# Kernel optimization log

Measured on AMD Instinct MI355X. Metric: run time of the kernel, lower is better.

Reference implementation:

```python
import jax, jax.numpy as jnp
import numpy as np

B, S, F = 4, 2048, 512
H, DK, DV, FILT = 8, 64, 64, 512

def setup_inputs() -> dict:
    key = jax.random.key(0)
    ks = jax.random.split(key, 11)
    sc_in = 1.0 / np.sqrt(F)
    sc_o = 1.0 / np.sqrt(H * DV)
    return {
        "x_q": jax.random.normal(ks[0], (B, S, F), jnp.float32),
        "x_k": jax.random.normal(ks[1], (B, S, F), jnp.float32),
        "x_v": jax.random.normal(ks[2], (B, S, F), jnp.float32),
        "Wq": jax.random.normal(ks[3], (H, F, DK), jnp.float32) * sc_in,
        "bq": jax.random.normal(ks[4], (H, DK), jnp.float32) * 0.01,
        "Wk": jax.random.normal(ks[5], (H, F, DK), jnp.float32) * sc_in,
        "bk": jax.random.normal(ks[6], (H, DK), jnp.float32) * 0.01,
        "Wv": jax.random.normal(ks[7], (H, F, DV), jnp.float32) * sc_in,
        "bv": jax.random.normal(ks[8], (H, DV), jnp.float32) * 0.01,
        "Wo": jax.random.normal(ks[9], (H * DV, FILT), jnp.float32) * sc_o,
        "bo": jax.random.normal(ks[10], (FILT,), jnp.float32) * 0.01,
    }

def reference(x_q, x_k, x_v, Wq, bq, Wk, bk, Wv, bv, Wo, bo):
    d_k = Wq.shape[-1]
    # per-head Dense projections, batched over heads: [B,H,S,dk/dv]
    q = jnp.einsum("bsf,hfk->bhsk", x_q, Wq) + bq[:, None, :]
    k = jnp.einsum("bsf,hfk->bhsk", x_k, Wk) + bk[:, None, :]
    v = jnp.einsum("bsf,hfv->bhsv", x_v, Wv) + bv[:, None, :]
    # scaled dot-product attention (scale by 1/sqrt(d_k) as in map_fn)
    scores = jnp.einsum("bhsk,bhtk->bhst", q, k) / jnp.sqrt(jnp.asarray(d_k, q.dtype))
    attn = jax.nn.softmax(scores, axis=-1)
    out = jnp.einsum("bhst,bhtv->bhsv", attn, v)
    # concat heads along feature dim -> [B,S,H*DV], then output linear
    bsz, h, s, dv = out.shape
    concat = out.transpose(0, 2, 1, 3).reshape(bsz, s, h * dv)
    return concat @ Wo + bo
```

## Files before the change

kernel.cpp:

```cpp
#include <hip/hip_runtime.h>

#define B_    4
#define S_    2048
#define H_    8
#define M_    (B_ * S_)

typedef __bf16    bf16_t;
typedef _Float16  f16_t;
typedef __bf16   bf16x8 __attribute__((ext_vector_type(8)));
typedef __bf16   bf16x4 __attribute__((ext_vector_type(4)));
typedef _Float16 f16x8  __attribute__((ext_vector_type(8)));
typedef float    f32x16 __attribute__((ext_vector_type(16)));

union B8 { uint4 u; bf16x8 v; bf16_t e[8]; };
union B4 { uint2 u; bf16x4 v; bf16_t e[4]; };
union H8 { uint4 u; f16x8  v; f16_t  e[8]; };
union H4 { uint2 u; f16_t  e[4]; };

#define QSCALE 0.1803368801111204f

typedef const __attribute__((address_space(1))) unsigned int ga_u32;
typedef __attribute__((address_space(3))) unsigned int       ls_u32;
__device__ __forceinline__ void g2l16(const void* g, void* l) {
    __builtin_amdgcn_global_load_lds((ga_u32*)g, (ls_u32*)l, 16, 0, 0);
}

__global__ __launch_bounds__(256) void prep(
    const float* __restrict__ xq, const float* __restrict__ xk,
    const float* __restrict__ xv,
    bf16_t* __restrict__ dq, bf16_t* __restrict__ dk, bf16_t* __restrict__ dv,
    const float* __restrict__ w0, const float* __restrict__ w1,
    const float* __restrict__ w2, const float* __restrict__ wo,
    bf16_t* __restrict__ t0, bf16_t* __restrict__ t1,
    bf16_t* __restrict__ t2, f16_t* __restrict__ wot)
{
    __shared__ float T[64][65];
    const int bid = blockIdx.x;
    const int tid = threadIdx.x;

    if (bid < 3072) {
        const int z  = bid >> 10;
        const int bx = bid & 1023;
        const float* src = z == 0 ? xq : z == 1 ? xk : xv;
        bf16_t*      dst = z == 0 ? dq : z == 1 ? dk : dv;
        const size_t base = (size_t)bx * 4096 + tid * 8;
        #pragma unroll
        for (int k = 0; k < 2; ++k) {
            const size_t i = base + (size_t)k * 2048;
            float4 a = *(const float4*)(src + i);
            float4 b = *(const float4*)(src + i + 4);
            B8 o;
            o.e[0] = (bf16_t)a.x; o.e[1] = (bf16_t)a.y;
            o.e[2] = (bf16_t)a.z; o.e[3] = (bf16_t)a.w;
            o.e[4] = (bf16_t)b.x; o.e[5] = (bf16_t)b.y;
            o.e[6] = (bf16_t)b.z; o.e[7] = (bf16_t)b.w;
            *(uint4*)(dst + i) = o.u;
        }
        return;
    }

    const int cid = bid - 3072;
    const int z   = cid >> 6;
    const int rem = cid & 63;
    const int k0  = (rem & 7) * 64;
    const int row = tid & 63, q4 = tid >> 6;

    if (z < 3) {
        const float* W  = z == 0 ? w0 : z == 1 ? w1 : w2;
        bf16_t*      Wt = z == 0 ? t0 : z == 1 ? t1 : t2;
        const int h = rem >> 3;
        const float* Wh = W + (size_t)h * 512 * 64;
        #pragma unroll
        for (int i = 0; i < 4; ++i) {
            int fq = q4 * 4 + i;
            float4 v = *(const float4*)(Wh + (size_t)(k0 + row) * 64 + fq * 4);
            T[row][fq * 4 + 0] = v.x; T[row][fq * 4 + 1] = v.y;
            T[row][fq * 4 + 2] = v.z; T[row][fq * 4 + 3] = v.w;
        }
        __syncthreads();
        bf16_t* Wth = Wt + (size_t)h * 64 * 512;
        #pragma unroll
        for (int i = 0; i < 4; ++i) {
            int kq = q4 * 4 + i;
            B4 o;
            #pragma unroll
            for (int j = 0; j < 4; ++j) o.e[j] = (bf16_t)T[kq * 4 + j][row];
            *(uint2*)(Wth + (size_t)row * 512 + k0 + kq * 4) = o.u;
        }
    } else {
        const int n0 = (rem >> 3) * 64;
        #pragma unroll
        for (int i = 0; i < 4; ++i) {
            int fq = q4 * 4 + i;
            float4 v = *(const float4*)(wo + (size_t)(k0 + row) * 512 + n0 + fq * 4);
            T[row][fq * 4 + 0] = v.x; T[row][fq * 4 + 1] = v.y;
            T[row][fq * 4 + 2] = v.z; T[row][fq * 4 + 3] = v.w;
        }
        __syncthreads();
        #pragma unroll
        for (int i = 0; i < 4; ++i) {
            int kq = q4 * 4 + i;
            H4 o;
            #pragma unroll
            for (int j = 0; j < 4; ++j) o.e[j] = (f16_t)T[kq * 4 + j][row];
            *(uint2*)(wot + (size_t)(n0 + row) * 512 + k0 + kq * 4) = o.u;
        }
    }
}

__global__ __launch_bounds__(256) void proj_tiled(
    const bf16_t* __restrict__ xq, const bf16_t* __restrict__ xk,
    const bf16_t* __restrict__ xv,
    const bf16_t* __restrict__ Wtq, const bf16_t* __restrict__ Wtk,
    const bf16_t* __restrict__ Wtv,
    const float* __restrict__ bq, const float* __restrict__ bk,
    const float* __restrict__ bv,
    bf16_t* __restrict__ Qb, bf16_t* __restrict__ Kb, bf16_t* __restrict__ Vt)
{
    __shared__ char sm[34816];
    bf16_t* As = (bf16_t*)sm;
    bf16_t* Bs = As + 128 * 64;

    const int z = blockIdx.z;
    const bf16_t* X    = z == 0 ? xq  : z == 1 ? xk  : xv;
    const bf16_t* Wt   = z == 0 ? Wtq : z == 1 ? Wtk : Wtv;
    const float*  bias = z == 0 ? bq  : z == 1 ? bk  : bv;

    const int tid  = threadIdx.x;
    const int wave = tid >> 6, lane = tid & 63;
    const int l31  = lane & 31, half = lane >> 5;
    const int m0   = blockIdx.x * 128;
    const int n0   = blockIdx.y * 128;
    const int mw   = (wave & 1) * 64;
    const int nw   = (wave >> 1) * 64;

    const int srow = lane >> 3;
    const int scol = (lane & 7) * 16;

    f32x16 acc[2][2];
    #pragma unroll
    for (int mt = 0; mt < 2; ++mt)
        #pragma unroll
        for (int nt = 0; nt < 2; ++nt)
            #pragma unroll
            for (int i = 0; i < 16; ++i) acc[mt][nt][i] = 0.0f;

    for (int k0 = 0; k0 < 512; k0 += 64) {
        __syncthreads();
        #pragma unroll
        for (int i = 0; i < 4; ++i) {
            const int inst = wave * 4 + i;
            const int row  = inst * 8 + srow;
            g2l16((const char*)X  + ((size_t)(m0 + row) * 512 + k0) * 2 + scol,
                  sm + inst * 1024);
            g2l16((const char*)Wt + ((size_t)(n0 + row) * 512 + k0) * 2 + scol,
                  sm + 16384 + inst * 1024);
        }
        __syncthreads();

        #pragma unroll
        for (int kc = 0; kc < 4; ++kc) {
            B8 a0, a1, b0, b1;
            a0.u = *(const uint4*)&As[(mw + l31)      * 64 + kc * 16 + half * 8];
            a1.u = *(const uint4*)&As[(mw + 32 + l31) * 64 + kc * 16 + half * 8];
            b0.u = *(const uint4*)&Bs[(nw + l31)      * 64 + kc * 16 + half * 8];
            b1.u = *(const uint4*)&Bs[(nw + 32 + l31) * 64 + kc * 16 + half * 8];
            acc[0][0] = __builtin_amdgcn_mfma_f32_32x32x16_bf16(a0.v, b0.v, acc[0][0], 0, 0, 0);
            acc[0][1] = __builtin_amdgcn_mfma_f32_32x32x16_bf16(a0.v, b1.v, acc[0][1], 0, 0, 0);
            acc[1][0] = __builtin_amdgcn_mfma_f32_32x32x16_bf16(a1.v, b0.v, acc[1][0], 0, 0, 0);
            acc[1][1] = __builtin_amdgcn_mfma_f32_32x32x16_bf16(a1.v, b1.v, acc[1][1], 0, 0, 0);
        }
    }

    if (z <= 1) {
        const float sc_ = (z == 0) ? QSCALE : 1.0f;
        bf16_t* Out = (z == 0) ? Qb : Kb;
        #pragma unroll
        for (int mt = 0; mt < 2; ++mt)
            #pragma unroll
            for (int nt = 0; nt < 2; ++nt) {
                int n = n0 + nw + nt * 32 + l31;
                float bv_ = bias[n];
                #pragma unroll
                for (int r = 0; r < 16; ++r) {
                    int m = m0 + mw + mt * 32 + (r & 3) + 8 * (r >> 2) + 4 * half;
                    Out[(size_t)m * 512 + n] = (bf16_t)((acc[mt][nt][r] + bv_) * sc_);
                }
            }
    } else {
        const int b  = m0 >> 11;
        const int sb = m0 & 2047;
        __syncthreads();
        #pragma unroll
        for (int mt = 0; mt < 2; ++mt)
            #pragma unroll
            for (int nt = 0; nt < 2; ++nt) {
                const int nl  = nw + nt * 32 + l31;
                const float bv_ = bias[n0 + nl];
                #pragma unroll
                for (int r = 0; r < 16; r += 2) {
                    const int ml = mw + mt * 32 + (r & 3) + 8 * (r >> 2) + 4 * half;
                    union { unsigned u; bf16_t e[2]; } pk;
                    pk.e[0] = (bf16_t)(acc[mt][nt][r]     + bv_);
                    pk.e[1] = (bf16_t)(acc[mt][nt][r + 1] + bv_);
                    *(unsigned*)(sm + nl * 272 + ml * 2) = pk.u;
                }
            }
        __syncthreads();
        const int dl16 = tid >> 4;
        const int cc   = tid & 15;
        #pragma unroll
        for (int p = 0; p < 8; ++p) {
            const int d_l = p * 16 + dl16;
            const int ng  = n0 + d_l;
            const int h   = ng >> 6, dd = ng & 63;
            uint4 val = *(const uint4*)(sm + d_l * 272 + cc * 16);
            *(uint4*)(Vt + ((size_t)((b * 8 + h) * 64 + dd)) * 2048 + sb + cc * 8) = val;
        }
    }
}

__global__ __launch_bounds__(512, 2) void attn_mfma(
    const bf16_t* __restrict__ Q, const bf16_t* __restrict__ K,
    const bf16_t* __restrict__ Vt, f16_t* __restrict__ O)
{
    __shared__ char smraw[73728];
    bf16_t* Ks = (bf16_t*)smraw;
    bf16_t* Vs = Ks + 4 * 64 * 72;

    const int bh  = blockIdx.y;
    const int b   = bh >> 3, h = bh & 7;
    const int q0  = blockIdx.x * 256;
    const int tid = threadIdx.x;
    const int wave = tid >> 6, lane = tid & 63;
    const int l31 = lane & 31, half = lane >> 5;
    const int qsub = wave & 3, ksplit = wave >> 2;

    bf16x8 qfA[4], qfB[4];
    {
        const bf16_t* qp = Q + ((size_t)(b * S_ + q0 + qsub * 64 + l31)) * 512 + h * 64 + half * 8;
        #pragma unroll
        for (int ks = 0; ks < 4; ++ks) {
            B8 t;
            t.u = *(const uint4*)(qp + ks * 16);              qfA[ks] = t.v;
            t.u = *(const uint4*)(qp + 32 * 512 + ks * 16);   qfB[ks] = t.v;
        }
    }

    f32x16 oA0, oA1, oB0, oB1;
    #pragma unroll
    for (int i = 0; i < 16; ++i) { oA0[i] = 0.0f; oA1[i] = 0.0f; oB0[i] = 0.0f; oB1[i] = 0.0f; }
    float lA = 0.0f, lB = 0.0f;

    const bf16_t* Kbase = K + ((size_t)b * S_) * 512 + h * 64;
    const bf16_t* Vbase = Vt + ((size_t)bh * 64) * 2048;

    const int sbuf = tid >> 8;
    const int p    = tid & 255;
    const int kr = p >> 3, kc8 = p & 7;
    const int vd = p >> 2, vj = p & 3;
    const int kqmap[4] = {0, 2, 1, 3};
    const int vkq = kqmap[vj];

    uint4 kreg0, kreg1;
    uint2 vreg[4];

#define LOADSET(TB) do {                                                      \
        kreg0 = *(const uint4*)(Kbase + (size_t)((TB) + kr) * 512 + kc8 * 8); \
        kreg1 = *(const uint4*)(Kbase + (size_t)((TB) + kr + 32) * 512 + kc8 * 8); \
        _Pragma("unroll")                                                     \
        for (int g = 0; g < 4; ++g)                                           \
            vreg[g] = *(const uint2*)(Vbase + (size_t)vd * 2048 + (TB) + g * 16 + vkq * 4); \
    } while (0)

#define WRITESET(SLOT) do {                                                   \
        bf16_t* KsS = Ks + ((SLOT) * 2 + sbuf) * 4608;                        \
        bf16_t* VsS = Vs + ((SLOT) * 2 + sbuf) * 4608;                        \
        *(uint4*)&KsS[kr * 72 + kc8 * 8]        = kreg0;                      \
        *(uint4*)&KsS[(kr + 32) * 72 + kc8 * 8] = kreg1;                      \
        _Pragma("unroll")                                                     \
        for (int g = 0; g < 4; ++g)                                           \
            *(uint2*)&VsS[vd * 72 + g * 16 + vj * 4] = vreg[g];               \
    } while (0)

    LOADSET(sbuf * 1024);
    WRITESET(0);
    LOADSET(sbuf * 1024 + 64);
    __syncthreads();

    for (int it = 0; it < 16; ++it) {
        const int slot = it & 1;
        if (it + 1 < 16) WRITESET(slot ^ 1);
        if (it + 2 < 16) LOADSET(sbuf * 1024 + (it + 2) * 64);

        const bf16_t* KsC = Ks + (slot * 2 + ksplit) * 4608;
        const bf16_t* VsC = Vs + (slot * 2 + ksplit) * 4608;

        f32x16 s00, s01, s10, s11;
        #pragma unroll
        for (int i = 0; i < 16; ++i) { s00[i] = 0.0f; s01[i] = 0.0f; s10[i] = 0.0f; s11[i] = 0.0f; }
        #pragma unroll
        for (int ks = 0; ks < 4; ++ks) {
            B8 kk0, kk1;
            kk0.u = *(const uint4*)(&KsC[l31 * 72 + ks * 16 + half * 8]);
            kk1.u = *(const uint4*)(&KsC[(32 + l31) * 72 + ks * 16 + half * 8]);
            s00 = __builtin_amdgcn_mfma_f32_32x32x16_bf16(kk0.v, qfA[ks], s00, 0, 0, 0);
            s01 = __builtin_amdgcn_mfma_f32_32x32x16_bf16(kk0.v, qfB[ks], s01, 0, 0, 0);
            s10 = __builtin_amdgcn_mfma_f32_32x32x16_bf16(kk1.v, qfA[ks], s10, 0, 0, 0);
            s11 = __builtin_amdgcn_mfma_f32_32x32x16_bf16(kk1.v, qfB[ks], s11, 0, 0, 0);
        }

        float lsA = 0.0f, lsB = 0.0f;
        #pragma unroll
        for (int r = 0; r < 16; ++r) {
            s00[r] = __builtin_amdgcn_exp2f(s00[r]); lsA += s00[r];
            s10[r] = __builtin_amdgcn_exp2f(s10[r]); lsA += s10[r];
            s01[r] = __builtin_amdgcn_exp2f(s01[r]); lsB += s01[r];
            s11[r] = __builtin_amdgcn_exp2f(s11[r]); lsB += s11[r];
        }
        lA += lsA; lB += lsB;

        B8 pfA[4], pfB[4];
        #pragma unroll
        for (int j = 0; j < 8; ++j) {
            pfA[0].e[j] = (bf16_t)s00[j];
            pfA[1].e[j] = (bf16_t)s00[8 + j];
            pfA[2].e[j] = (bf16_t)s10[j];
            pfA[3].e[j] = (bf16_t)s10[8 + j];
            pfB[0].e[j] = (bf16_t)s01[j];
            pfB[1].e[j] = (bf16_t)s01[8 + j];
            pfB[2].e[j] = (bf16_t)s11[j];
            pfB[3].e[j] = (bf16_t)s11[8 + j];
        }

        #pragma unroll
        for (int c = 0; c < 4; ++c) {
            B8 va, vb;
            va.u = *(const uint4*)(&VsC[l31 * 72 + c * 16 + half * 8]);
            vb.u = *(const uint4*)(&VsC[(32 + l31) * 72 + c * 16 + half * 8]);
            oA0 = __builtin_amdgcn_mfma_f32_32x32x16_bf16(va.v, pfA[c].v, oA0, 0, 0, 0);
            oA1 = __builtin_amdgcn_mfma_f32_32x32x16_bf16(vb.v, pfA[c].v, oA1, 0, 0, 0);
            oB0 = __builtin_amdgcn_mfma_f32_32x32x16_bf16(va.v, pfB[c].v, oB0, 0, 0, 0);
            oB1 = __builtin_amdgcn_mfma_f32_32x32x16_bf16(vb.v, pfB[c].v, oB1, 0, 0, 0);
        }

        __syncthreads();
    }
#undef LOADSET
#undef WRITESET

    lA += __shfl_xor(lA, 32);
    lB += __shfl_xor(lB, 32);
    __syncthreads();
    float* co = (float*)smraw;
    float* cl = co + 4 * 64 * 68;
    if (ksplit == 1) {
        float* reg = co + qsub * (64 * 68);
        #pragma unroll
        for (int r = 0; r < 16; ++r) {
            reg[r * 68 + lane]        = oA0[r];
            reg[(16 + r) * 68 + lane] = oA1[r];
            reg[(32 + r) * 68 + lane] = oB0[r];
            reg[(48 + r) * 68 + lane] = oB1[r];
        }
        cl[qsub * 128 + lane]      = lA;
        cl[qsub * 128 + 64 + lane] = lB;
    }
    __syncthreads();
    if (ksplit == 0) {
        float* reg = co + qsub * (64 * 68);
        float invA = 1.0f / (lA + cl[qsub * 128 + lane]);
        float invB = 1.0f / (lB + cl[qsub * 128 + 64 + lane]);
        f16_t* ObA = O + ((size_t)(b * S_ + q0 + qsub * 64 + l31)) * 512 + h * 64;
        f16_t* ObB = ObA + (size_t)32 * 512;
        #pragma unroll
        for (int g = 0; g < 4; ++g) {
            H4 a, c, e, f;
            #pragma unroll
            for (int j = 0; j < 4; ++j) {
                int r = g * 4 + j;
                a.e[j] = (f16_t)((oA0[r] + reg[r * 68 + lane])        * invA);
                c.e[j] = (f16_t)((oA1[r] + reg[(16 + r) * 68 + lane]) * invA);
                e.e[j] = (f16_t)((oB0[r] + reg[(32 + r) * 68 + lane]) * invB);
                f.e[j] = (f16_t)((oB1[r] + reg[(48 + r) * 68 + lane]) * invB);
            }
            int d = 8 * g + 4 * half;
            *(uint2*)(ObA + d)      = a.u;
            *(uint2*)(ObA + 32 + d) = c.u;
            *(uint2*)(ObB + d)      = e.u;
            *(uint2*)(ObB + 32 + d) = f.u;
        }
    }
}

__global__ __launch_bounds__(256) void gemm_out_tiled(
    const f16_t* __restrict__ A, const f16_t* __restrict__ Wot,
    const float* __restrict__ bias, float* __restrict__ C)
{
    __shared__ f16_t As[64 * 72];
    __shared__ f16_t Bs[64 * 72];

    const int tid  = threadIdx.x;
    const int wave = tid >> 6, lane = tid & 63;
    const int l31  = lane & 31, half = lane >> 5;
    const int m0   = blockIdx.x * 64;
    const int n0   = blockIdx.y * 64;
    const int mw   = (wave & 1) * 32;
    const int nw   = (wave >> 1) * 32;

    const int sr  = tid >> 2;
    const int so  = (tid & 3) * 16;

    uint4 pA0, pA1, pB0, pB1;
    {
        const f16_t* ap = A   + (size_t)(m0 + sr) * 512 + so;
        const f16_t* bp = Wot + (size_t)(n0 + sr) * 512 + so;
        pA0 = *(const uint4*)(ap); pA1 = *(const uint4*)(ap + 8);
        pB0 = *(const uint4*)(bp); pB1 = *(const uint4*)(bp + 8);
    }

    f32x16 acc;
    #pragma unroll
    for (int i = 0; i < 16; ++i) acc[i] = 0.0f;

    for (int k0 = 0; k0 < 512; k0 += 64) {
        __syncthreads();
        *(uint4*)&As[sr * 72 + so]     = pA0;
        *(uint4*)&As[sr * 72 + so + 8] = pA1;
        *(uint4*)&Bs[sr * 72 + so]     = pB0;
        *(uint4*)&Bs[sr * 72 + so + 8] = pB1;
        __syncthreads();
        if (k0 + 64 < 512) {
            const f16_t* ap = A   + (size_t)(m0 + sr) * 512 + k0 + 64 + so;
            const f16_t* bp = Wot + (size_t)(n0 + sr) * 512 + k0 + 64 + so;
            pA0 = *(const uint4*)(ap); pA1 = *(const uint4*)(ap + 8);
            pB0 = *(const uint4*)(bp); pB1 = *(const uint4*)(bp + 8);
        }

        #pragma unroll
        for (int kc = 0; kc < 4; ++kc) {
            H8 a, b;
            a.u = *(const uint4*)&As[(mw + l31) * 72 + kc * 16 + half * 8];
            b.u = *(const uint4*)&Bs[(nw + l31) * 72 + kc * 16 + half * 8];
            acc = __builtin_amdgcn_mfma_f32_32x32x16_f16(a.v, b.v, acc, 0, 0, 0);
        }
    }

    const int n = n0 + nw + l31;
    const float bias0 = bias[n];
    #pragma unroll
    for (int r = 0; r < 16; ++r) {
        int m = m0 + mw + (r & 3) + 8 * (r >> 2) + 4 * half;
        C[(size_t)m * 512 + n] = acc[r] + bias0;
    }
}

extern "C" void kernel_launch(void* const* d_in, const int* in_sizes, int n_in,
                              void* d_out, int out_size, void* d_ws, size_t ws_size,
                              hipStream_t stream)
{
    const float* x_q = (const float*)d_in[0];
    const float* x_k = (const float*)d_in[1];
    const float* x_v = (const float*)d_in[2];
    const float* Wq  = (const float*)d_in[3];
    const float* bq  = (const float*)d_in[4];
    const float* Wk  = (const float*)d_in[5];
    const float* bk  = (const float*)d_in[6];
    const float* Wv  = (const float*)d_in[7];
    const float* bv  = (const float*)d_in[8];
    const float* Wo  = (const float*)d_in[9];
    const float* bo  = (const float*)d_in[10];
    float* out = (float*)d_out;

    char* W = (char*)d_ws;
    bf16_t* Wtq = (bf16_t*)W;
    bf16_t* Wtk = Wtq + (size_t)8 * 64 * 512;
    bf16_t* Wtv = Wtk + (size_t)8 * 64 * 512;
    f16_t*  Wot = (f16_t*)(Wtv + (size_t)8 * 64 * 512);
    bf16_t* Qb  = (bf16_t*)(Wot + (size_t)512 * 512);
    bf16_t* Kb  = Qb + (size_t)M_ * 512;
    bf16_t* Vt  = Kb + (size_t)M_ * 512;
    f16_t*  AO  = (f16_t*)(Vt + (size_t)M_ * 512);

    bf16_t* Xqb = (bf16_t*)out;
    bf16_t* Xkb = Xqb + (size_t)M_ * 512;
    bf16_t* Xvb = (bf16_t*)AO;

    prep<<<dim3(3328), 256, 0, stream>>>(
        x_q, x_k, x_v, Xqb, Xkb, Xvb,
        Wq, Wk, Wv, Wo, Wtq, Wtk, Wtv, Wot);

    proj_tiled<<<dim3(64, 4, 3), 256, 0, stream>>>(
        Xqb, Xkb, Xvb, Wtq, Wtk, Wtv, bq, bk, bv, Qb, Kb, Vt);

    attn_mfma<<<dim3(S_ / 256, B_ * H_), 512, 0, stream>>>(Qb, Kb, Vt, AO);

    gemm_out_tiled<<<dim3(128, 8), 256, 0, stream>>>(AO, Wot, bo, out);
}
```

Measured before the change: 201.0 us.

## Stage K/V tiles via direct global-to-LDS loads instead of register staging

Replaces the register-staged K/V prefetch (global load into registers, later store to padded LDS) with global_load_lds 16-byte direct transfers into unpadded 64-wide LDS tiles. It removes the register round trip and VGPR pressure, and shrinks the pipeline from two tiles ahead to one. V fragment reads are split into two 8-byte loads to match the new layout. Dropping the padding risks LDS bank conflicts, and the shorter prefetch distance can expose more global latency.

```diff
diff --git a/kernel.cpp b/kernel.cpp
--- a/kernel.cpp
+++ b/kernel.cpp
@@ -224,9 +224,9 @@
     const bf16_t* __restrict__ Q, const bf16_t* __restrict__ K,
     const bf16_t* __restrict__ Vt, f16_t* __restrict__ O)
 {
-    __shared__ char smraw[73728];
+    __shared__ char smraw[71680];
     bf16_t* Ks = (bf16_t*)smraw;
-    bf16_t* Vs = Ks + 4 * 64 * 72;
+    bf16_t* Vs = Ks + 4 * 64 * 64;
 
     const int bh  = blockIdx.y;
     const int b   = bh >> 3, h = bh & 7;
@@ -235,6 +235,8 @@
     const int wave = tid >> 6, lane = tid & 63;
     const int l31 = lane & 31, half = lane >> 5;
     const int qsub = wave & 3, ksplit = wave >> 2;
+    const int lrow = lane >> 3;
+    const int lcol = (lane & 7) * 16;
 
     bf16x8 qfA[4], qfB[4];
     {
@@ -252,49 +254,37 @@
     for (int i = 0; i < 16; ++i) { oA0[i] = 0.0f; oA1[i] = 0.0f; oB0[i] = 0.0f; oB1[i] = 0.0f; }
     float lA = 0.0f, lB = 0.0f;
 
-    const bf16_t* Kbase = K + ((size_t)b * S_) * 512 + h * 64;
-    const bf16_t* Vbase = Vt + ((size_t)bh * 64) * 2048;
-
-    const int sbuf = tid >> 8;
-    const int p    = tid & 255;
-    const int kr = p >> 3, kc8 = p & 7;
-    const int vd = p >> 2, vj = p & 3;
-    const int kqmap[4] = {0, 2, 1, 3};
-    const int vkq = kqmap[vj];
-
-    uint4 kreg0, kreg1;
-    uint2 vreg[4];
-
-#define LOADSET(TB) do {                                                      \
-        kreg0 = *(const uint4*)(Kbase + (size_t)((TB) + kr) * 512 + kc8 * 8); \
-        kreg1 = *(const uint4*)(Kbase + (size_t)((TB) + kr + 32) * 512 + kc8 * 8); \
+    const char* Kb_b = (const char*)(K + ((size_t)b * S_) * 512 + h * 64);
+    const char* Vb_b = (const char*)(Vt + ((size_t)bh * 64) * 2048);
+
+#define STAGE(SLOT, TB) do {                                                  \
         _Pragma("unroll")                                                     \
-        for (int g = 0; g < 4; ++g)                                           \
-            vreg[g] = *(const uint2*)(Vbase + (size_t)vd * 2048 + (TB) + g * 16 + vkq * 4); \
+        for (int i_ = 0; i_ < 4; ++i_) {                                      \
+            const int j_   = wave * 4 + i_;                                   \
+            const int kind = j_ >> 3;                                         \
+            const int ksb  = kind & 1;                                        \
+            const int sub  = j_ & 7;                                          \
+            if (kind < 2) {                                                   \
+                const int key = (TB) + ksb * 1024 + sub * 8 + lrow;           \
+                g2l16(Kb_b + (size_t)key * 1024 + lcol,                       \
+                      (char*)(Ks + ((SLOT) * 2 + ksb) * 4096) + sub * 1024);  \
+            } else {                                                          \
+                const int dd = sub * 8 + lrow;                                \
+                g2l16(Vb_b + (size_t)dd * 4096 + ((TB) + ksb * 1024) * 2 + lcol, \
+                      (char*)(Vs + ((SLOT) * 2 + ksb) * 4096) + sub * 1024);  \
+            }                                                                 \
+        }                                                                     \
     } while (0)
 
-#define WRITESET(SLOT) do {                                                   \
-        bf16_t* KsS = Ks + ((SLOT) * 2 + sbuf) * 4608;                        \
-        bf16_t* VsS = Vs + ((SLOT) * 2 + sbuf) * 4608;                        \
-        *(uint4*)&KsS[kr * 72 + kc8 * 8]        = kreg0;                      \
-        *(uint4*)&KsS[(kr + 32) * 72 + kc8 * 8] = kreg1;                      \
-        _Pragma("unroll")                                                     \
-        for (int g = 0; g < 4; ++g)                                           \
-            *(uint2*)&VsS[vd * 72 + g * 16 + vj * 4] = vreg[g];               \
-    } while (0)
-
-    LOADSET(sbuf * 1024);
-    WRITESET(0);
-    LOADSET(sbuf * 1024 + 64);
+    STAGE(0, 0);
     __syncthreads();
 
     for (int it = 0; it < 16; ++it) {
         const int slot = it & 1;
-        if (it + 1 < 16) WRITESET(slot ^ 1);
-        if (it + 2 < 16) LOADSET(sbuf * 1024 + (it + 2) * 64);
-
-        const bf16_t* KsC = Ks + (slot * 2 + ksplit) * 4608;
-        const bf16_t* VsC = Vs + (slot * 2 + ksplit) * 4608;
+        if (it + 1 < 16) STAGE(slot ^ 1, (it + 1) * 64);
+
+        const bf16_t* KsC = Ks + (slot * 2 + ksplit) * 4096;
+        const bf16_t* VsC = Vs + (slot * 2 + ksplit) * 4096;
 
         f32x16 s00, s01, s10, s11;
         #pragma unroll
@@ -302,8 +292,8 @@
         #pragma unroll
         for (int ks = 0; ks < 4; ++ks) {
             B8 kk0, kk1;
-            kk0.u = *(const uint4*)(&KsC[l31 * 72 + ks * 16 + half * 8]);
-            kk1.u = *(const uint4*)(&KsC[(32 + l31) * 72 + ks * 16 + half * 8]);
+            kk0.u = *(const uint4*)(&KsC[l31 * 64 + ks * 16 + half * 8]);
+            kk1.u = *(const uint4*)(&KsC[(32 + l31) * 64 + ks * 16 + half * 8]);
             s00 = __builtin_amdgcn_mfma_f32_32x32x16_bf16(kk0.v, qfA[ks], s00, 0, 0, 0);
             s01 = __builtin_amdgcn_mfma_f32_32x32x16_bf16(kk0.v, qfB[ks], s01, 0, 0, 0);
             s10 = __builtin_amdgcn_mfma_f32_32x32x16_bf16(kk1.v, qfA[ks], s10, 0, 0, 0);
@@ -336,8 +326,10 @@
         #pragma unroll
         for (int c = 0; c < 4; ++c) {
             B8 va, vb;
-            va.u = *(const uint4*)(&VsC[l31 * 72 + c * 16 + half * 8]);
-            vb.u = *(const uint4*)(&VsC[(32 + l31) * 72 + c * 16 + half * 8]);
+            *(uint2*)&va.e[0] = *(const uint2*)(&VsC[l31 * 64 + c * 16 + half * 4]);
+            *(uint2*)&va.e[4] = *(const uint2*)(&VsC[l31 * 64 + c * 16 + 8 + half * 4]);
+            *(uint2*)&vb.e[0] = *(const uint2*)(&VsC[(32 + l31) * 64 + c * 16 + half * 4]);
+            *(uint2*)&vb.e[4] = *(const uint2*)(&VsC[(32 + l31) * 64 + c * 16 + 8 + half * 4]);
             oA0 = __builtin_amdgcn_mfma_f32_32x32x16_bf16(va.v, pfA[c].v, oA0, 0, 0, 0);
             oA1 = __builtin_amdgcn_mfma_f32_32x32x16_bf16(vb.v, pfA[c].v, oA1, 0, 0, 0);
             oB0 = __builtin_amdgcn_mfma_f32_32x32x16_bf16(va.v, pfB[c].v, oB0, 0, 0, 0);
@@ -346,8 +338,7 @@
 
         __syncthreads();
     }
-#undef LOADSET
-#undef WRITESET
+#undef STAGE
 
     lA += __shfl_xor(lA, 32);
     lB += __shfl_xor(lB, 32);
```

Measured after the change: 239.8 us. 19.3% more time.
